# Kernel tuning notes

Measured on AMD Instinct MI355X. Metric: run time of the kernel, lower is better.

Reference implementation:

```python
import jax, jax.numpy as jnp
import numpy as np

NUM_PAGES = 1048576
TOKENS_PER_PAGE = 32
SLOTS = 256
MAX_PAGES_PER_SLOT = 4096
MAX_SEQ = 65536  # <= max_pages_per_slot*tokens_per_page/2, leaves room to grow


def setup_inputs() -> dict:
    key = jax.random.key(0)
    k1, = jax.random.split(key, 1)
    # random current sequence lengths per slot (some may be 0 / inactive)
    seq = jax.random.randint(k1, (SLOTS,), 0, MAX_SEQ).astype(jnp.int32)
    npu = (seq + TOKENS_PER_PAGE - 1) // TOKENS_PER_PAGE  # ceil-div pages used
    cols = jnp.arange(MAX_PAGES_PER_SLOT, dtype=jnp.int32)
    # give slot i the disjoint page-id range [1 + i*2048, ...); valid since
    # max pages/slot here = ceil(65535/32) = 2048 and 1+255*2048+2047 < NUM_PAGES
    pm = jnp.where(
        cols[None, :] < npu[:, None],
        1 + jnp.arange(SLOTS, dtype=jnp.int32)[:, None] * 2048 + cols[None, :],
        -1,
    ).astype(jnp.int32)
    # mark exactly the mapped pages as in-use (index 0 used as a safe dump slot)
    safe_idx = jnp.where(pm > -1, pm, 0)
    vals = (pm > -1).astype(jnp.int32)
    page_status = jnp.zeros((NUM_PAGES,), jnp.int32).at[safe_idx].max(vals)
    page_status = page_status.at[0].set(0)
    current_page = jnp.where(
        npu > 0,
        jnp.take_along_axis(pm, jnp.maximum(npu - 1, 0)[:, None], axis=1)[:, 0],
        -1,
    ).astype(jnp.int32)
    cpp = jnp.where(seq == 0, 0, (seq - 1) % TOKENS_PER_PAGE).astype(jnp.int32)
    return {
        "page_status": page_status,
        "page_map": pm,
        "sequence_lengths": seq,
        "num_pages_used": npu.astype(jnp.int32),
        "current_page": current_page,
        "current_page_position": cpp,
    }


def _find_next_free_page(page_status):
    # matches PageManager.find_next_free_page: first free index in [1, N), else 0
    free = jnp.where(page_status[1:] == 0, size=1, fill_value=-1)[0] + 1
    return free[0].astype(jnp.int32)


def reference(page_status, page_map, sequence_lengths, num_pages_used,
              current_page, current_page_position):
    """Faithful port of PageManager.reserve_decode_step_pages (autoregressive step)."""
    tpp = TOKENS_PER_PAGE
    new_seq = sequence_lengths + jnp.where(current_page == -1, 0, 1).astype(jnp.int32)
    new_npu = (new_seq + tpp - 1) // tpp
    new_cpp = jnp.where(new_seq == 0, 0, (new_seq - 1) % tpp).astype(jnp.int32)

    def step(carry, i):
        ps, pm, cp = carry
        needs_new_page = new_npu[i] > num_pages_used[i]
        nfp = jax.lax.cond(
            needs_new_page,
            lambda: _find_next_free_page(ps),
            lambda: jnp.int32(-1),
        )
        ps = jax.lax.cond(needs_new_page, lambda x: x.at[nfp].set(1), lambda x: x, ps)
        pm = jax.lax.cond(
            needs_new_page,
            lambda x: x.at[i, num_pages_used[i]].set(nfp),
            lambda x: x,
            pm,
        )
        cp = jax.lax.cond(needs_new_page, lambda x: x.at[i].set(nfp), lambda x: x, cp)
        return (ps, pm, cp), None

    (ps, pm, cp), _ = jax.lax.scan(
        step, (page_status, page_map, current_page), jnp.arange(SLOTS, dtype=jnp.int32)
    )
    # PageState fields in declaration order
    return (ps, pm, new_seq, new_npu.astype(jnp.int32), cp, new_cpp)
```

## Files before the change

kernel.cpp:

```cpp
#include <hip/hip_runtime.h>

#define NUM_PAGES 1048576
#define TPP 32
#define SLOTS 256
#define MPPS 4096
#define NBLK 1024
#define NTHR 256

__global__ __launch_bounds__(NTHR) void fused(
    const int* __restrict__ ps, const int* __restrict__ pm,
    const int* __restrict__ seq, const int* __restrict__ npu,
    const int* __restrict__ cp, int* __restrict__ out)
{
    const int t = threadIdx.x, b = blockIdx.x;
    const int lane = t & 63, wave = t >> 6;
    const unsigned long long mlt = (1ULL << lane) - 1ULL;

    int* out_ps  = out;
    int* out_pm  = out + NUM_PAGES;
    int* out_seq = out + 2 * NUM_PAGES;
    int* out_npu = out_seq + SLOTS;
    int* out_cp  = out_npu + SLOTS;
    int* out_cpp = out_cp + SLOTS;

    __shared__ int s_w[4];
    __shared__ int s_free[SLOTS];
    __shared__ int s_found;

    const int4* ps4 = reinterpret_cast<const int4*>(ps);

    const int gi = b * NTHR + t;
    const int4 pv = ps4[gi];
    const int4 mv = reinterpret_cast<const int4*>(pm)[gi];
    const int4 pc0 = ps4[t];
    const int4 pc1 = ps4[NTHR + t];
    const int4 pc2 = ps4[2 * NTHR + t];
    const int sq = seq[t], c = cp[t], u = npu[t];

    reinterpret_cast<int4*>(out_ps)[gi] = pv;
    reinterpret_cast<int4*>(out_pm)[gi] = mv;

    int ns = sq + (c != -1);
    int nn = (ns + TPP - 1) / TPP;
    int ncpp = (ns == 0) ? 0 : ((ns - 1) & (TPP - 1));
    int needs = (nn > u) ? 1 : 0;
    unsigned long long bal = __ballot(needs);
    if (lane == 0) s_w[wave] = __popcll(bal);
    if (t == 0) s_found = 0;
    __syncthreads();
    int woff = 0;
    for (int w = 0; w < wave; ++w) woff += s_w[w];
    const int r = woff + __popcll(bal & mlt);
    const int K = s_w[0] + s_w[1] + s_w[2] + s_w[3];
    if (b == 0) {
        out_seq[t] = ns;
        out_npu[t] = nn;
        out_cpp[t] = ncpp;
    }
    __syncthreads();

    auto process = [&](int4 v, int ch) {
        int m = ((v.x == 0) ? 1 : 0) | ((v.y == 0) ? 2 : 0) |
                ((v.z == 0) ? 4 : 0) | ((v.w == 0) ? 8 : 0);
        if (ch == 0 && t == 0) m &= ~1;
        int q = __popc(m);
        int x = q;
        for (int o = 1; o < 64; o <<= 1) { int y = __shfl_up(x, o); if (lane >= o) x += y; }
        if (lane == 63) s_w[wave] = x;
        int sf = s_found;
        __syncthreads();
        int wo = 0;
        for (int w = 0; w < wave; ++w) wo += s_w[w];
        int pos = sf + wo + x - q;
        #pragma unroll
        for (int j = 0; j < 4; ++j) if (m & (1 << j)) {
            int p = pos + __popc(m & ((1 << j) - 1));
            if (p < K) s_free[p] = ch * 1024 + t * 4 + j;
        }
        if (t == 0) s_found = sf + s_w[0] + s_w[1] + s_w[2] + s_w[3];
        __syncthreads();
    };

    process(pc0, 0);
    if (s_found < K) process(pc1, 1);
    if (s_found < K) process(pc2, 2);
    for (int ch = 3; ch < NBLK && s_found < K; ++ch)
        process(ps4[ch * NTHR + t], ch);

    const int fe = (s_found < K) ? s_found : K;

    const int nfp = (needs && r < fe) ? s_free[r] : 0;
    if (b == 0) out_cp[t] = needs ? nfp : c;
    if (needs && t == (b >> 2) && (u >> 10) == (b & 3))
        out_pm[t * MPPS + u] = nfp;
    if (t < K) {
        int f = (t < fe) ? s_free[t] : 0;
        if ((f >> 10) == b) out_ps[f] = 1;
    }
}

extern "C" void kernel_launch(void* const* d_in, const int* in_sizes, int n_in,
                              void* d_out, int out_size, void* d_ws, size_t ws_size,
                              hipStream_t stream)
{
    const int* page_status = (const int*)d_in[0];
    const int* page_map    = (const int*)d_in[1];
    const int* seq         = (const int*)d_in[2];
    const int* npu         = (const int*)d_in[3];
    const int* cp          = (const int*)d_in[4];

    fused<<<NBLK, NTHR, 0, stream>>>(
        page_status, page_map, seq, npu, cp, (int*)d_out);
}
```

Before: 10.50 us.

## Halve grid size and merge page updates into register copy before store

The grid shrinks from 1024 to 512 blocks, and each block copies two int4 chunks of page_status and page_map. Newly allocated page ids and status flags are now patched into the register copies before the vectorized stores, instead of being written as separate scattered stores after the bulk copy. This removes the ordering problem of overwriting copied data and the extra small global writes. In exchange each block carries more registers and shared arrays, and every block still repeats the redundant free-page scan.

```diff
diff --git a/kernel.cpp b/kernel.cpp
--- a/kernel.cpp
+++ b/kernel.cpp
@@ -4,7 +4,7 @@
 #define TPP 32
 #define SLOTS 256
 #define MPPS 4096
-#define NBLK 1024
+#define NBLK 512
 #define NTHR 256
 
 __global__ __launch_bounds__(NTHR) void fused(
@@ -25,40 +25,42 @@
 
     __shared__ int s_w[4];
     __shared__ int s_free[SLOTS];
+    __shared__ int s_nfp[SLOTS];
+    __shared__ int s_col[SLOTS];
     __shared__ int s_found;
 
     const int4* ps4 = reinterpret_cast<const int4*>(ps);
 
-    const int gi = b * NTHR + t;
-    const int4 pv = ps4[gi];
-    const int4 mv = reinterpret_cast<const int4*>(pm)[gi];
+    const int gi0 = b * (2 * NTHR) + t;
+    const int gi1 = gi0 + NTHR;
+    int4 pv0 = ps4[gi0];
+    int4 pv1 = ps4[gi1];
+    int4 mv0 = reinterpret_cast<const int4*>(pm)[gi0];
+    int4 mv1 = reinterpret_cast<const int4*>(pm)[gi1];
     const int4 pc0 = ps4[t];
     const int4 pc1 = ps4[NTHR + t];
     const int4 pc2 = ps4[2 * NTHR + t];
     const int sq = seq[t], c = cp[t], u = npu[t];
 
-    reinterpret_cast<int4*>(out_ps)[gi] = pv;
-    reinterpret_cast<int4*>(out_pm)[gi] = mv;
-
     int ns = sq + (c != -1);
     int nn = (ns + TPP - 1) / TPP;
-    int ncpp = (ns == 0) ? 0 : ((ns - 1) & (TPP - 1));
     int needs = (nn > u) ? 1 : 0;
     unsigned long long bal = __ballot(needs);
     if (lane == 0) s_w[wave] = __popcll(bal);
     if (t == 0) s_found = 0;
+    if (b == 0) {
+        out_seq[t] = ns;
+        out_npu[t] = nn;
+        out_cpp[t] = (ns == 0) ? 0 : ((ns - 1) & (TPP - 1));
+    }
     __syncthreads();
     int woff = 0;
     for (int w = 0; w < wave; ++w) woff += s_w[w];
     const int r = woff + __popcll(bal & mlt);
     const int K = s_w[0] + s_w[1] + s_w[2] + s_w[3];
-    if (b == 0) {
-        out_seq[t] = ns;
-        out_npu[t] = nn;
-        out_cpp[t] = ncpp;
-    }
     __syncthreads();
 
+    int pmask0 = 0, pmask1 = 0;
     auto process = [&](int4 v, int ch) {
         int m = ((v.x == 0) ? 1 : 0) | ((v.y == 0) ? 2 : 0) |
                 ((v.z == 0) ? 4 : 0) | ((v.w == 0) ? 8 : 0);
@@ -75,7 +77,11 @@
         #pragma unroll
         for (int j = 0; j < 4; ++j) if (m & (1 << j)) {
             int p = pos + __popc(m & ((1 << j) - 1));
-            if (p < K) s_free[p] = ch * 1024 + t * 4 + j;
+            if (p < K) {
+                s_free[p] = ch * 1024 + t * 4 + j;
+                if (ch == 2 * b)     pmask0 |= 1 << j;
+                if (ch == 2 * b + 1) pmask1 |= 1 << j;
+            }
         }
         if (t == 0) s_found = sf + s_w[0] + s_w[1] + s_w[2] + s_w[3];
         __syncthreads();
@@ -84,19 +90,43 @@
     process(pc0, 0);
     if (s_found < K) process(pc1, 1);
     if (s_found < K) process(pc2, 2);
-    for (int ch = 3; ch < NBLK && s_found < K; ++ch)
+    for (int ch = 3; ch < NUM_PAGES / 1024 && s_found < K; ++ch)
         process(ps4[ch * NTHR + t], ch);
 
     const int fe = (s_found < K) ? s_found : K;
 
     const int nfp = (needs && r < fe) ? s_free[r] : 0;
+    s_nfp[t] = needs ? nfp : -1;
+    s_col[t] = u;
     if (b == 0) out_cp[t] = needs ? nfp : c;
-    if (needs && t == (b >> 2) && (u >> 10) == (b & 3))
-        out_pm[t * MPPS + u] = nfp;
-    if (t < K) {
-        int f = (t < fe) ? s_free[t] : 0;
-        if ((f >> 10) == b) out_ps[f] = 1;
+    if (fe < K && b == 0 && t == 0) pmask0 |= 1;
+    __syncthreads();
+
+    {
+        int s0 = gi0 >> 10, p0 = s_nfp[s0];
+        if (p0 != -1) {
+            int d = s_col[s0] - ((gi0 & 1023) << 2);
+            if ((unsigned)d < 4u) reinterpret_cast<int*>(&mv0)[d] = p0;
+        }
+        int s1 = gi1 >> 10, p1 = s_nfp[s1];
+        if (p1 != -1) {
+            int d = s_col[s1] - ((gi1 & 1023) << 2);
+            if ((unsigned)d < 4u) reinterpret_cast<int*>(&mv1)[d] = p1;
+        }
     }
+    if (pmask0 & 1) pv0.x = 1;
+    if (pmask0 & 2) pv0.y = 1;
+    if (pmask0 & 4) pv0.z = 1;
+    if (pmask0 & 8) pv0.w = 1;
+    if (pmask1 & 1) pv1.x = 1;
+    if (pmask1 & 2) pv1.y = 1;
+    if (pmask1 & 4) pv1.z = 1;
+    if (pmask1 & 8) pv1.w = 1;
+
+    reinterpret_cast<int4*>(out_ps)[gi0] = pv0;
+    reinterpret_cast<int4*>(out_ps)[gi1] = pv1;
+    reinterpret_cast<int4*>(out_pm)[gi0] = mv0;
+    reinterpret_cast<int4*>(out_pm)[gi1] = mv1;
 }
 
 extern "C" void kernel_launch(void* const* d_in, const int* in_sizes, int n_in,
```

Result: slower. 35.31 us (+236.3%).
